# Kernel optimization log

Hardware: AMD Instinct MI355X
Metric: run time of the kernel (lower is better)

## Reference

```python
import jax, jax.numpy as jnp
from jax import lax
import numpy as np


def setup_inputs() -> dict:
    key = jax.random.key(0)
    ks = jax.random.split(key, 5)
    B, T, I, H, L = 64, 512, 1024, 1024, 1
    stdv = 1.0 / (H ** 0.5)
    return {
        "input": jax.random.normal(ks[0], (B, T, I), dtype=jnp.float32),
        "weight_ih": jax.random.uniform(ks[1], (L, H, I), jnp.float32, -stdv, stdv),
        "weight_hh": jax.random.uniform(ks[2], (L, H, H), jnp.float32, -stdv, stdv),
        "bias_ih": jax.random.uniform(ks[3], (L, H), jnp.float32, -stdv, stdv),
        "bias_hh": jax.random.uniform(ks[4], (L, H), jnp.float32, -stdv, stdv),
    }


def reference(input, weight_ih, weight_hh, bias_ih, bias_hh):
    # input: (B, T, I); weights per layer; hx: (L, B, H)
    L, H, I = weight_ih.shape
    B, T, _ = input.shape
    h0 = jnp.zeros((L, B, H), dtype=input.dtype)
    bias = (bias_ih + bias_hh)[:, None, :]  # (L, 1, H)
    # Hoist the input projection out of the recurrence: one big GEMM.
    x_proj = jnp.einsum("bti,lhi->tlbh", input, weight_ih)  # (T, L, B, H)

    def step(h, xp):
        # h: (L, B, H); per-layer recurrent matmul
        g = xp + jnp.einsum("lbh,lgh->lbg", h, weight_hh) + bias
        h_new = jnp.tanh(g)
        return h_new, h_new

    h_last, outs = lax.scan(step, h0, x_proj)  # outs: (T, L, B, H)
    output = jnp.transpose(outs, (1, 0, 2, 3))  # (L, T, B, H) matching torch cat(dim=1)
    return output, h_last
```

## Files before the change

### kernel.cpp

```cpp
#include <hip/hip_runtime.h>
#include <hip/hip_bf16.h>
#include <stdint.h>

#define B_ 64
#define T_ 512
#define I_ 1024
#define H_ 1024
#define BH (B_*H_)

typedef __attribute__((ext_vector_type(8))) short short8;
typedef __attribute__((ext_vector_type(4))) float f32x4;
typedef __attribute__((ext_vector_type(4))) unsigned u32x4;
typedef __attribute__((ext_vector_type(2))) unsigned u32x2;

static __device__ __forceinline__ unsigned short f2bf(float f) {
  union { float f; unsigned u; } v; v.f = f;
  unsigned r = v.u + 0x7fffu + ((v.u >> 16) & 1u);
  return (unsigned short)(r >> 16);
}

static __device__ __forceinline__ void glds16(const void* g, void* l) {
  __builtin_amdgcn_global_load_lds(
      (const __attribute__((address_space(1))) unsigned int*)g,
      (__attribute__((address_space(3))) unsigned int*)l, 16, 0, 0);
}

__global__ void convert_weights(const f32x4* __restrict__ wih, const f32x4* __restrict__ whh,
                                uint2* __restrict__ wih_b, uint2* __restrict__ whh_b)
{
  int idx = blockIdx.x * blockDim.x + threadIdx.x;
  f32x4 a = wih[idx];
  uint2 o;
  o.x = f2bf(a[0]) | ((unsigned)f2bf(a[1]) << 16);
  o.y = f2bf(a[2]) | ((unsigned)f2bf(a[3]) << 16);
  wih_b[idx] = o;
  f32x4 b = whh[idx];
  uint2 p;
  p.x = f2bf(b[0]) | ((unsigned)f2bf(b[1]) << 16);
  p.y = f2bf(b[2]) | ((unsigned)f2bf(b[3]) << 16);
  whh_b[idx] = p;
}

__launch_bounds__(256)
__global__ void gemm_xproj(const float* __restrict__ in,
                           const unsigned short* __restrict__ wb,
                           const float* __restrict__ bih,
                           const float* __restrict__ bhh,
                           float* __restrict__ out)
{
  __shared__ __align__(16) unsigned char As[16384];
  __shared__ __align__(16) unsigned char Bs[16384];
  const int tid = threadIdx.x;
  const int lane = tid & 63;
  const int w = tid >> 6;
  const int wm = w >> 1, wn = w & 1;
  const int bn = blockIdx.x, bm = blockIdx.y;

  const int ar = tid >> 1;
  const int ah = tid & 1;
  const int R0 = bm*128 + ar;
  const float* asrc = in + (size_t)(R0 & 63) * (T_*I_) + (size_t)(R0 >> 6) * I_ + ah*32;
  unsigned char* adst_base = As + ar*128;
  const int aswz_w = (ar & 7) << 4;

  f32x4 acc[4][4];
  #pragma unroll
  for (int i = 0; i < 4; ++i)
    #pragma unroll
    for (int j = 0; j < 4; ++j)
      acc[i][j] = (f32x4){0.f,0.f,0.f,0.f};

  f32x4 av[8];
  #pragma unroll
  for (int j = 0; j < 8; ++j) av[j] = *(const f32x4*)(asrc + 0*64 + j*4);

  for (int kt = 0; kt < 16; ++kt) {
    __syncthreads();
    #pragma unroll
    for (int q = 0; q < 4; ++q) {
      int inst = w*4 + q;
      int rb = inst*8 + (lane >> 3);
      int srcoff = ((bn*128 + rb) * I_ + kt*64) * 2 + (((lane & 7) * 16) ^ ((rb & 7) << 4));
      glds16((const unsigned char*)wb + srcoff, Bs + inst*1024);
    }
    #pragma unroll
    for (int j2 = 0; j2 < 4; ++j2) {
      uint4 val;
      f32x4 v0 = av[j2*2], v1 = av[j2*2+1];
      val.x = f2bf(v0[0]) | ((unsigned)f2bf(v0[1]) << 16);
      val.y = f2bf(v0[2]) | ((unsigned)f2bf(v0[3]) << 16);
      val.z = f2bf(v1[0]) | ((unsigned)f2bf(v1[1]) << 16);
      val.w = f2bf(v1[2]) | ((unsigned)f2bf(v1[3]) << 16);
      int koffb = ah*64 + j2*16;
      *(uint4*)(adst_base + (koffb ^ aswz_w)) = val;
    }
    __syncthreads();
    if (kt < 15) {
      #pragma unroll
      for (int j = 0; j < 8; ++j) av[j] = *(const f32x4*)(asrc + (kt+1)*64 + j*4);
    }
    #pragma unroll
    for (int kb = 0; kb < 2; ++kb) {
      const int kby = kb*64 + ((lane >> 4) << 4);
      short8 af[4], bfr[4];
      #pragma unroll
      for (int i = 0; i < 4; ++i) {
        int ra = wm*64 + i*16 + (lane & 15);
        af[i] = *(const short8*)(As + ra*128 + (kby ^ ((ra & 7) << 4)));
      }
      #pragma unroll
      for (int j = 0; j < 4; ++j) {
        int rb2 = wn*64 + j*16 + (lane & 15);
        bfr[j] = *(const short8*)(Bs + rb2*128 + (kby ^ ((rb2 & 7) << 4)));
      }
      #pragma unroll
      for (int i = 0; i < 4; ++i)
        #pragma unroll
        for (int j = 0; j < 4; ++j)
          acc[i][j] = __builtin_amdgcn_mfma_f32_16x16x32_bf16(af[i], bfr[j], acc[i][j], 0, 0, 0);
    }
  }
  #pragma unroll
  for (int j = 0; j < 4; ++j) {
    int col = bn*128 + wn*64 + j*16 + (lane & 15);
    float bias = bih[col] + bhh[col];
    #pragma unroll
    for (int i = 0; i < 4; ++i) {
      int Rb = bm*128 + wm*64 + i*16 + ((lane >> 4) << 2);
      #pragma unroll
      for (int q = 0; q < 4; ++q) {
        int R = Rb + q;
        out[(size_t)(R >> 6) * BH + (size_t)(R & 63) * H_ + col] = acc[i][j][q] + bias;
      }
    }
  }
}

__launch_bounds__(256, 1)
__global__ void rnn_recur(const unsigned short* __restrict__ whh_b,
                          float* __restrict__ out,
                          unsigned char* __restrict__ hx)
{
  extern __shared__ __align__(16) unsigned char lds[];
  const int tid = threadIdx.x;
  const int lane = tid & 63;
  const int w = tid >> 6;
  const int g = blockIdx.x;
  const int gb = g >> 4;
  const int gn = g & 15;

  for (int q = 0; q < 32; ++q) {
    int inst = w*32 + q;
    int nl = inst >> 1;
    int koff = (inst & 1)*1024 + lane*16;
    size_t srcoff = (size_t)(gn*64 + nl)*2048 + (size_t)(koff ^ ((nl & 7) << 4));
    glds16((const unsigned char*)whh_b + srcoff, lds + inst*1024);
  }
  asm volatile("s_waitcnt vmcnt(0)" ::: "memory");
  __syncthreads();

  const int arow = w*16 + (lane & 15);
  const unsigned char* wsrow = lds + (size_t)arow*2048;
  const int aswz = (arow & 7) << 4;
  const int klane = (lane >> 4) << 4;
  short8 af[32];
  #pragma unroll
  for (int kb = 0; kb < 32; ++kb)
    af[kb] = *(const short8*)(wsrow + ((kb*64 + klane) ^ aswz));
  __syncthreads();

  const int bb = lane & 15;
  const int nq = (lane >> 4) << 2;
  const int colb = gn*64 + w*16 + nq;
  const int brow = gb*16 + bb;
  const int bswz = (bb & 7) << 4;

  const int srow = tid & 15;
  const int scol = tid >> 4;
  const int sswz = (srow & 7) << 4;

  f32x4 xp = *(const f32x4*)(out + (size_t)brow*H_ + colb);

  for (int t = 0; t < T_; ++t) {
    unsigned char* hsb = lds + (size_t)(t & 1)*32768;
    unsigned char* sdst = hsb + srow*2048;
    if (t == 0) {
      u32x2 z = (u32x2){0u, 0u};
      #pragma unroll
      for (int j = 0; j < 16; ++j)
        *(u32x2*)(sdst + (((j*16 + scol)*8) ^ sswz)) = z;
    } else {
      const unsigned want = (unsigned)t;
      const unsigned char* pb = hx + (size_t)(t & 1)*262144 + (size_t)gb*65536 + (size_t)tid*16;
      u32x4 v0,v1,v2,v3,v4,v5,v6,v7,v8,v9,v10,v11,v12,v13,v14,v15;
      for (;;) {
        asm volatile(
          "global_load_dwordx4 %0, %8, off sc0 sc1\n\t"
          "global_load_dwordx4 %1, %9, off sc0 sc1\n\t"
          "global_load_dwordx4 %2, %10, off sc0 sc1\n\t"
          "global_load_dwordx4 %3, %11, off sc0 sc1\n\t"
          "global_load_dwordx4 %4, %12, off sc0 sc1\n\t"
          "global_load_dwordx4 %5, %13, off sc0 sc1\n\t"
          "global_load_dwordx4 %6, %14, off sc0 sc1\n\t"
          "global_load_dwordx4 %7, %15, off sc0 sc1"
          : "=&v"(v0),"=&v"(v1),"=&v"(v2),"=&v"(v3),"=&v"(v4),"=&v"(v5),"=&v"(v6),"=&v"(v7)
          : "v"(pb), "v"(pb+4096), "v"(pb+2*4096), "v"(pb+3*4096),
            "v"(pb+4*4096), "v"(pb+5*4096), "v"(pb+6*4096), "v"(pb+7*4096)
          : "memory");
        asm volatile(
          "global_load_dwordx4 %0, %8, off sc0 sc1\n\t"
          "global_load_dwordx4 %1, %9, off sc0 sc1\n\t"
          "global_load_dwordx4 %2, %10, off sc0 sc1\n\t"
          "global_load_dwordx4 %3, %11, off sc0 sc1\n\t"
          "global_load_dwordx4 %4, %12, off sc0 sc1\n\t"
          "global_load_dwordx4 %5, %13, off sc0 sc1\n\t"
          "global_load_dwordx4 %6, %14, off sc0 sc1\n\t"
          "global_load_dwordx4 %7, %15, off sc0 sc1"
          : "=&v"(v8),"=&v"(v9),"=&v"(v10),"=&v"(v11),"=&v"(v12),"=&v"(v13),"=&v"(v14),"=&v"(v15)
          : "v"(pb+8*4096), "v"(pb+9*4096), "v"(pb+10*4096), "v"(pb+11*4096),
            "v"(pb+12*4096), "v"(pb+13*4096), "v"(pb+14*4096), "v"(pb+15*4096)
          : "memory");
        asm volatile("s_waitcnt vmcnt(0)"
          : "+v"(v0),"+v"(v1),"+v"(v2),"+v"(v3),"+v"(v4),"+v"(v5),"+v"(v6),"+v"(v7),
            "+v"(v8),"+v"(v9),"+v"(v10),"+v"(v11),"+v"(v12),"+v"(v13),"+v"(v14),"+v"(v15)
          :: "memory");
        int ok = 1;
        #define CHK(vv, jj) if ((jj) != gn && vv[2] != want) ok = 0;
        CHK(v0,0)  CHK(v1,1)  CHK(v2,2)  CHK(v3,3)
        CHK(v4,4)  CHK(v5,5)  CHK(v6,6)  CHK(v7,7)
        CHK(v8,8)  CHK(v9,9)  CHK(v10,10) CHK(v11,11)
        CHK(v12,12) CHK(v13,13) CHK(v14,14) CHK(v15,15)
        #undef CHK
        if (ok) break;
        __builtin_amdgcn_s_sleep(1);
      }
      #define STG(vv, jj) if ((jj) != gn) \
        *(u32x2*)(sdst + ((((jj)*16 + scol)*8) ^ sswz)) = (u32x2){vv[0], vv[1]};
      STG(v0,0)  STG(v1,1)  STG(v2,2)  STG(v3,3)
      STG(v4,4)  STG(v5,5)  STG(v6,6)  STG(v7,7)
      STG(v8,8)  STG(v9,9)  STG(v10,10) STG(v11,11)
      STG(v12,12) STG(v13,13) STG(v14,14) STG(v15,15)
      #undef STG
    }
    asm volatile("s_waitcnt lgkmcnt(0)\n\ts_barrier" ::: "memory");

    const unsigned char* hfrow = hsb + (size_t)bb*2048;
    f32x4 acc0 = (f32x4){0.f,0.f,0.f,0.f}, acc1 = (f32x4){0.f,0.f,0.f,0.f};
    #pragma unroll
    for (int kb = 0; kb < 32; kb += 2) {
      short8 b0 = *(const short8*)(hfrow + ((kb*64 + klane) ^ bswz));
      short8 b1 = *(const short8*)(hfrow + (((kb+1)*64 + klane) ^ bswz));
      acc0 = __builtin_amdgcn_mfma_f32_16x16x32_bf16(af[kb],   b0, acc0, 0, 0, 0);
      acc1 = __builtin_amdgcn_mfma_f32_16x16x32_bf16(af[kb+1], b1, acc1, 0, 0, 0);
    }
    f32x4 hval;
    #pragma unroll
    for (int q = 0; q < 4; ++q)
      hval[q] = tanhf(acc0[q] + acc1[q] + xp[q]);

    u32x4 pkt;
    pkt[0] = f2bf(hval[0]) | ((unsigned)f2bf(hval[1]) << 16);
    pkt[1] = f2bf(hval[2]) | ((unsigned)f2bf(hval[3]) << 16);
    pkt[2] = (unsigned)(t + 1);
    pkt[3] = 0u;
    const unsigned char* wp = hx + (size_t)((t+1) & 1)*262144 + (size_t)gb*65536
                              + (size_t)(gn*256 + tid)*16;
    asm volatile("global_store_dwordx4 %0, %1, off sc0 sc1" :: "v"(wp), "v"(pkt) : "memory");

    unsigned char* hsn = lds + (size_t)((t+1) & 1)*32768;
    *(u32x2*)(hsn + (size_t)bb*2048 + ((colb*2) ^ bswz)) = (u32x2){pkt[0], pkt[1]};

    *(f32x4*)(out + (size_t)t*BH + (size_t)brow*H_ + colb) = hval;
    if (t == T_-1)
      *(f32x4*)(out + (size_t)T_*BH + (size_t)brow*H_ + colb) = hval;

    int tn = (t < T_-1) ? t+1 : t;
    xp = *(const f32x4*)(out + (size_t)tn*BH + (size_t)brow*H_ + colb);
  }
}

extern "C" void kernel_launch(void* const* d_in, const int* in_sizes, int n_in,
                              void* d_out, int out_size, void* d_ws, size_t ws_size,
                              hipStream_t stream)
{
  const float* in  = (const float*)d_in[0];
  const float* wih = (const float*)d_in[1];
  const float* whh = (const float*)d_in[2];
  const float* bih = (const float*)d_in[3];
  const float* bhh = (const float*)d_in[4];
  float* out = (float*)d_out;
  unsigned char* ws = (unsigned char*)d_ws;

  unsigned char*  hx    = ws;
  unsigned short* wih_b = (unsigned short*)(ws + 524288);
  unsigned short* whh_b = (unsigned short*)(ws + 524288 + 2097152);

  hipMemsetAsync(hx, 0, 524288, stream);
  convert_weights<<<1024, 256, 0, stream>>>((const f32x4*)wih, (const f32x4*)whh,
                                            (uint2*)wih_b, (uint2*)whh_b);
  gemm_xproj<<<dim3(8, 256), 256, 0, stream>>>(in, wih_b, bih, bhh, out);
  rnn_recur<<<64, 256, 131072, stream>>>(whh_b, out, hx);
}
```

Measured before the change: 1.768 ms.

## Pre-convert input to bf16, use async LDS loads in GEMM, refine recurrence polling

Adds a separate pass that converts the fp32 input to bf16 in (t,b)-row order, so the projection GEMM can stage both operands with direct global-to-LDS loads and drop the in-loop fp32 conversion. The recurrence's spin-wait now sleeps briefly before the first poll and then reloads only the slices that are not ready yet, instead of reloading all sixteen. Each block's own slice now comes back through global memory rather than a local LDS write. The recurrent matmul is split over four accumulators instead of two to give more MFMA independence. In exchange there is an extra pass over the input with a bf16 buffer written and read back, plus a fixed sleep on every timestep.

```diff
diff --git a/kernel.cpp b/kernel.cpp
--- a/kernel.cpp
+++ b/kernel.cpp
@@ -41,8 +41,26 @@
   whh_b[idx] = p;
 }
 
+__global__ void convert_input(const float* __restrict__ in, unsigned short* __restrict__ inb)
+{
+  size_t idx = (size_t)blockIdx.x * 256 + threadIdx.x;
+  size_t base = idx * 8;
+  size_t R = base >> 10;
+  int i = (int)(base & 1023);
+  int b = (int)(R & 63), t = (int)(R >> 6);
+  const float* src = in + ((size_t)b * T_ + (size_t)t) * I_ + i;
+  f32x4 x0 = *(const f32x4*)src;
+  f32x4 x1 = *(const f32x4*)(src + 4);
+  uint4 o;
+  o.x = f2bf(x0[0]) | ((unsigned)f2bf(x0[1]) << 16);
+  o.y = f2bf(x0[2]) | ((unsigned)f2bf(x0[3]) << 16);
+  o.z = f2bf(x1[0]) | ((unsigned)f2bf(x1[1]) << 16);
+  o.w = f2bf(x1[2]) | ((unsigned)f2bf(x1[3]) << 16);
+  *(uint4*)(inb + base) = o;
+}
+
 __launch_bounds__(256)
-__global__ void gemm_xproj(const float* __restrict__ in,
+__global__ void gemm_xproj(const unsigned short* __restrict__ inb,
                            const unsigned short* __restrict__ wb,
                            const float* __restrict__ bih,
                            const float* __restrict__ bhh,
@@ -56,13 +74,6 @@
   const int wm = w >> 1, wn = w & 1;
   const int bn = blockIdx.x, bm = blockIdx.y;
 
-  const int ar = tid >> 1;
-  const int ah = tid & 1;
-  const int R0 = bm*128 + ar;
-  const float* asrc = in + (size_t)(R0 & 63) * (T_*I_) + (size_t)(R0 >> 6) * I_ + ah*32;
-  unsigned char* adst_base = As + ar*128;
-  const int aswz_w = (ar & 7) << 4;
-
   f32x4 acc[4][4];
   #pragma unroll
   for (int i = 0; i < 4; ++i)
@@ -70,35 +81,18 @@
     for (int j = 0; j < 4; ++j)
       acc[i][j] = (f32x4){0.f,0.f,0.f,0.f};
 
-  f32x4 av[8];
-  #pragma unroll
-  for (int j = 0; j < 8; ++j) av[j] = *(const f32x4*)(asrc + 0*64 + j*4);
-
   for (int kt = 0; kt < 16; ++kt) {
     __syncthreads();
     #pragma unroll
     for (int q = 0; q < 4; ++q) {
       int inst = w*4 + q;
-      int rb = inst*8 + (lane >> 3);
-      int srcoff = ((bn*128 + rb) * I_ + kt*64) * 2 + (((lane & 7) * 16) ^ ((rb & 7) << 4));
-      glds16((const unsigned char*)wb + srcoff, Bs + inst*1024);
-    }
-    #pragma unroll
-    for (int j2 = 0; j2 < 4; ++j2) {
-      uint4 val;
-      f32x4 v0 = av[j2*2], v1 = av[j2*2+1];
-      val.x = f2bf(v0[0]) | ((unsigned)f2bf(v0[1]) << 16);
-      val.y = f2bf(v0[2]) | ((unsigned)f2bf(v0[3]) << 16);
-      val.z = f2bf(v1[0]) | ((unsigned)f2bf(v1[1]) << 16);
-      val.w = f2bf(v1[2]) | ((unsigned)f2bf(v1[3]) << 16);
-      int koffb = ah*64 + j2*16;
-      *(uint4*)(adst_base + (koffb ^ aswz_w)) = val;
+      int rr = inst*8 + (lane >> 3);
+      int soA = ((bm*128 + rr) * I_ + kt*64) * 2 + (((lane & 7) * 16) ^ ((rr & 7) << 4));
+      int soB = ((bn*128 + rr) * I_ + kt*64) * 2 + (((lane & 7) * 16) ^ ((rr & 7) << 4));
+      glds16((const unsigned char*)inb + soA, As + inst*1024);
+      glds16((const unsigned char*)wb  + soB, Bs + inst*1024);
     }
     __syncthreads();
-    if (kt < 15) {
-      #pragma unroll
-      for (int j = 0; j < 8; ++j) av[j] = *(const f32x4*)(asrc + (kt+1)*64 + j*4);
-    }
     #pragma unroll
     for (int kb = 0; kb < 2; ++kb) {
       const int kby = kb*64 + ((lane >> 4) << 4);
@@ -193,48 +187,66 @@
       const unsigned want = (unsigned)t;
       const unsigned char* pb = hx + (size_t)(t & 1)*262144 + (size_t)gb*65536 + (size_t)tid*16;
       u32x4 v0,v1,v2,v3,v4,v5,v6,v7,v8,v9,v10,v11,v12,v13,v14,v15;
-      for (;;) {
-        asm volatile(
-          "global_load_dwordx4 %0, %8, off sc0 sc1\n\t"
-          "global_load_dwordx4 %1, %9, off sc0 sc1\n\t"
-          "global_load_dwordx4 %2, %10, off sc0 sc1\n\t"
-          "global_load_dwordx4 %3, %11, off sc0 sc1\n\t"
-          "global_load_dwordx4 %4, %12, off sc0 sc1\n\t"
-          "global_load_dwordx4 %5, %13, off sc0 sc1\n\t"
-          "global_load_dwordx4 %6, %14, off sc0 sc1\n\t"
-          "global_load_dwordx4 %7, %15, off sc0 sc1"
-          : "=&v"(v0),"=&v"(v1),"=&v"(v2),"=&v"(v3),"=&v"(v4),"=&v"(v5),"=&v"(v6),"=&v"(v7)
-          : "v"(pb), "v"(pb+4096), "v"(pb+2*4096), "v"(pb+3*4096),
-            "v"(pb+4*4096), "v"(pb+5*4096), "v"(pb+6*4096), "v"(pb+7*4096)
-          : "memory");
-        asm volatile(
-          "global_load_dwordx4 %0, %8, off sc0 sc1\n\t"
-          "global_load_dwordx4 %1, %9, off sc0 sc1\n\t"
-          "global_load_dwordx4 %2, %10, off sc0 sc1\n\t"
-          "global_load_dwordx4 %3, %11, off sc0 sc1\n\t"
-          "global_load_dwordx4 %4, %12, off sc0 sc1\n\t"
-          "global_load_dwordx4 %5, %13, off sc0 sc1\n\t"
-          "global_load_dwordx4 %6, %14, off sc0 sc1\n\t"
-          "global_load_dwordx4 %7, %15, off sc0 sc1"
-          : "=&v"(v8),"=&v"(v9),"=&v"(v10),"=&v"(v11),"=&v"(v12),"=&v"(v13),"=&v"(v14),"=&v"(v15)
-          : "v"(pb+8*4096), "v"(pb+9*4096), "v"(pb+10*4096), "v"(pb+11*4096),
-            "v"(pb+12*4096), "v"(pb+13*4096), "v"(pb+14*4096), "v"(pb+15*4096)
-          : "memory");
+      __builtin_amdgcn_s_sleep(8);
+      asm volatile(
+        "global_load_dwordx4 %0, %8, off sc0 sc1\n\t"
+        "global_load_dwordx4 %1, %9, off sc0 sc1\n\t"
+        "global_load_dwordx4 %2, %10, off sc0 sc1\n\t"
+        "global_load_dwordx4 %3, %11, off sc0 sc1\n\t"
+        "global_load_dwordx4 %4, %12, off sc0 sc1\n\t"
+        "global_load_dwordx4 %5, %13, off sc0 sc1\n\t"
+        "global_load_dwordx4 %6, %14, off sc0 sc1\n\t"
+        "global_load_dwordx4 %7, %15, off sc0 sc1"
+        : "=&v"(v0),"=&v"(v1),"=&v"(v2),"=&v"(v3),"=&v"(v4),"=&v"(v5),"=&v"(v6),"=&v"(v7)
+        : "v"(pb), "v"(pb+4096), "v"(pb+2*4096), "v"(pb+3*4096),
+          "v"(pb+4*4096), "v"(pb+5*4096), "v"(pb+6*4096), "v"(pb+7*4096)
+        : "memory");
+      asm volatile(
+        "global_load_dwordx4 %0, %8, off sc0 sc1\n\t"
+        "global_load_dwordx4 %1, %9, off sc0 sc1\n\t"
+        "global_load_dwordx4 %2, %10, off sc0 sc1\n\t"
+        "global_load_dwordx4 %3, %11, off sc0 sc1\n\t"
+        "global_load_dwordx4 %4, %12, off sc0 sc1\n\t"
+        "global_load_dwordx4 %5, %13, off sc0 sc1\n\t"
+        "global_load_dwordx4 %6, %14, off sc0 sc1\n\t"
+        "global_load_dwordx4 %7, %15, off sc0 sc1"
+        : "=&v"(v8),"=&v"(v9),"=&v"(v10),"=&v"(v11),"=&v"(v12),"=&v"(v13),"=&v"(v14),"=&v"(v15)
+        : "v"(pb+8*4096), "v"(pb+9*4096), "v"(pb+10*4096), "v"(pb+11*4096),
+          "v"(pb+12*4096), "v"(pb+13*4096), "v"(pb+14*4096), "v"(pb+15*4096)
+        : "memory");
+      asm volatile("s_waitcnt vmcnt(0)"
+        : "+v"(v0),"+v"(v1),"+v"(v2),"+v"(v3),"+v"(v4),"+v"(v5),"+v"(v6),"+v"(v7),
+          "+v"(v8),"+v"(v9),"+v"(v10),"+v"(v11),"+v"(v12),"+v"(v13),"+v"(v14),"+v"(v15)
+        :: "memory");
+      unsigned m;
+      #define MKMASK() { m = 0; \
+        m |= (v0[2]==want)  ? 1u<<0  : 0u;  m |= (v1[2]==want)  ? 1u<<1  : 0u; \
+        m |= (v2[2]==want)  ? 1u<<2  : 0u;  m |= (v3[2]==want)  ? 1u<<3  : 0u; \
+        m |= (v4[2]==want)  ? 1u<<4  : 0u;  m |= (v5[2]==want)  ? 1u<<5  : 0u; \
+        m |= (v6[2]==want)  ? 1u<<6  : 0u;  m |= (v7[2]==want)  ? 1u<<7  : 0u; \
+        m |= (v8[2]==want)  ? 1u<<8  : 0u;  m |= (v9[2]==want)  ? 1u<<9  : 0u; \
+        m |= (v10[2]==want) ? 1u<<10 : 0u;  m |= (v11[2]==want) ? 1u<<11 : 0u; \
+        m |= (v12[2]==want) ? 1u<<12 : 0u;  m |= (v13[2]==want) ? 1u<<13 : 0u; \
+        m |= (v14[2]==want) ? 1u<<14 : 0u;  m |= (v15[2]==want) ? 1u<<15 : 0u; }
+      MKMASK()
+      while (m != 0xffffu) {
+        __builtin_amdgcn_s_sleep(1);
+        #define RLD(vv, jj) if (!((m >> (jj)) & 1u)) \
+          asm volatile("global_load_dwordx4 %0, %1, off sc0 sc1" \
+                       : "=&v"(vv) : "v"(pb + (jj)*4096) : "memory");
+        RLD(v0,0)  RLD(v1,1)  RLD(v2,2)  RLD(v3,3)
+        RLD(v4,4)  RLD(v5,5)  RLD(v6,6)  RLD(v7,7)
+        RLD(v8,8)  RLD(v9,9)  RLD(v10,10) RLD(v11,11)
+        RLD(v12,12) RLD(v13,13) RLD(v14,14) RLD(v15,15)
+        #undef RLD
         asm volatile("s_waitcnt vmcnt(0)"
           : "+v"(v0),"+v"(v1),"+v"(v2),"+v"(v3),"+v"(v4),"+v"(v5),"+v"(v6),"+v"(v7),
             "+v"(v8),"+v"(v9),"+v"(v10),"+v"(v11),"+v"(v12),"+v"(v13),"+v"(v14),"+v"(v15)
           :: "memory");
-        int ok = 1;
-        #define CHK(vv, jj) if ((jj) != gn && vv[2] != want) ok = 0;
-        CHK(v0,0)  CHK(v1,1)  CHK(v2,2)  CHK(v3,3)
-        CHK(v4,4)  CHK(v5,5)  CHK(v6,6)  CHK(v7,7)
-        CHK(v8,8)  CHK(v9,9)  CHK(v10,10) CHK(v11,11)
-        CHK(v12,12) CHK(v13,13) CHK(v14,14) CHK(v15,15)
-        #undef CHK
-        if (ok) break;
-        __builtin_amdgcn_s_sleep(1);
+        MKMASK()
       }
-      #define STG(vv, jj) if ((jj) != gn) \
+      #undef MKMASK
+      #define STG(vv, jj) \
         *(u32x2*)(sdst + ((((jj)*16 + scol)*8) ^ sswz)) = (u32x2){vv[0], vv[1]};
       STG(v0,0)  STG(v1,1)  STG(v2,2)  STG(v3,3)
       STG(v4,4)  STG(v5,5)  STG(v6,6)  STG(v7,7)
@@ -245,18 +257,22 @@
     asm volatile("s_waitcnt lgkmcnt(0)\n\ts_barrier" ::: "memory");
 
     const unsigned char* hfrow = hsb + (size_t)bb*2048;
-    f32x4 acc0 = (f32x4){0.f,0.f,0.f,0.f}, acc1 = (f32x4){0.f,0.f,0.f,0.f};
-    #pragma unroll
-    for (int kb = 0; kb < 32; kb += 2) {
+    f32x4 acc0 = (f32x4){0.f,0.f,0.f,0.f}, acc1 = acc0, acc2 = acc0, acc3 = acc0;
+    #pragma unroll
+    for (int kb = 0; kb < 32; kb += 4) {
       short8 b0 = *(const short8*)(hfrow + ((kb*64 + klane) ^ bswz));
       short8 b1 = *(const short8*)(hfrow + (((kb+1)*64 + klane) ^ bswz));
+      short8 b2 = *(const short8*)(hfrow + (((kb+2)*64 + klane) ^ bswz));
+      short8 b3 = *(const short8*)(hfrow + (((kb+3)*64 + klane) ^ bswz));
       acc0 = __builtin_amdgcn_mfma_f32_16x16x32_bf16(af[kb],   b0, acc0, 0, 0, 0);
       acc1 = __builtin_amdgcn_mfma_f32_16x16x32_bf16(af[kb+1], b1, acc1, 0, 0, 0);
+      acc2 = __builtin_amdgcn_mfma_f32_16x16x32_bf16(af[kb+2], b2, acc2, 0, 0, 0);
+      acc3 = __builtin_amdgcn_mfma_f32_16x16x32_bf16(af[kb+3], b3, acc3, 0, 0, 0);
     }
     f32x4 hval;
     #pragma unroll
     for (int q = 0; q < 4; ++q)
-      hval[q] = tanhf(acc0[q] + acc1[q] + xp[q]);
+      hval[q] = tanhf((acc0[q] + acc1[q]) + (acc2[q] + acc3[q]) + xp[q]);
 
     u32x4 pkt;
     pkt[0] = f2bf(hval[0]) | ((unsigned)f2bf(hval[1]) << 16);
@@ -267,9 +283,6 @@
                               + (size_t)(gn*256 + tid)*16;
     asm volatile("global_store_dwordx4 %0, %1, off sc0 sc1" :: "v"(wp), "v"(pkt) : "memory");
 
-    unsigned char* hsn = lds + (size_t)((t+1) & 1)*32768;
-    *(u32x2*)(hsn + (size_t)bb*2048 + ((colb*2) ^ bswz)) = (u32x2){pkt[0], pkt[1]};
-
     *(f32x4*)(out + (size_t)t*BH + (size_t)brow*H_ + colb) = hval;
     if (t == T_-1)
       *(f32x4*)(out + (size_t)T_*BH + (size_t)brow*H_ + colb) = hval;
@@ -294,10 +307,12 @@
   unsigned char*  hx    = ws;
   unsigned short* wih_b = (unsigned short*)(ws + 524288);
   unsigned short* whh_b = (unsigned short*)(ws + 524288 + 2097152);
+  unsigned short* inb   = (unsigned short*)(ws + 524288 + 4194304);
 
   hipMemsetAsync(hx, 0, 524288, stream);
   convert_weights<<<1024, 256, 0, stream>>>((const f32x4*)wih, (const f32x4*)whh,
                                             (uint2*)wih_b, (uint2*)whh_b);
-  gemm_xproj<<<dim3(8, 256), 256, 0, stream>>>(in, wih_b, bih, bhh, out);
+  convert_input<<<16384, 256, 0, stream>>>(in, inb);
+  gemm_xproj<<<dim3(8, 256), 256, 0, stream>>>(inb, whh_b == 0 ? 0 : wih_b, bih, bhh, out);
   rnn_recur<<<64, 256, 131072, stream>>>(whh_b, out, hx);
 }
```

After: 1.556 ms. 12.0% less time.
